# Optimization experiments

Hardware: AMD Instinct MI355X
Metric: run time of the kernel (lower is better)

## Reference

```python
import jax, jax.numpy as jnp
import numpy as np

B = 64        # number of graph segments
BASE = 384    # mean verts per segment
LMAX = 512    # pad length (counts in [256, 512])
H_DIM = 256
H_DIV = 128   # h_dim // h_dim_div
HEADS = 4
DH = H_DIV // HEADS  # 32


def _counts(seed):
    rng = np.random.default_rng(seed)
    d = rng.integers(-128, 129, B)
    d[1::2] = -d[::2]            # paired so the total is exactly B*BASE
    return (BASE + d).astype(np.int64)


def _pad_indices(counts, L):
    # Gather indices/mask mapping packed ragged tokens -> padded [B, L].
    counts = np.asarray(counts)
    off = np.concatenate([[0], np.cumsum(counts)[:-1]])
    ar = np.arange(L)[None, :]
    mask = ar < counts[:, None]
    idx = np.where(mask, off[:, None] + ar, 0)
    return idx, mask


def setup_inputs() -> dict:
    key = jax.random.key(0)
    ks = jax.random.split(key, 16)
    src_num_verts = _counts(0)
    dst_num_verts = _counts(1)
    total = B * BASE  # 24576 for both src and dst

    def w(k, shape):
        return 0.02 * jax.random.normal(k, shape, jnp.float32)

    return {
        'src_h': jax.random.normal(ks[0], (total, H_DIM), jnp.float32),
        'dst_h': jax.random.normal(ks[1], (total, H_DIM), jnp.float32),
        'src_num_verts': src_num_verts,
        'dst_num_verts': dst_num_verts,
        # 1x1 Conv1d == linear over channels
        'Wq': w(ks[2], (H_DIV, H_DIM)), 'bq': w(ks[3], (H_DIV,)),
        'Wk': w(ks[4], (H_DIV, H_DIM)), 'bk': w(ks[5], (H_DIV,)),
        'Wv': w(ks[6], (H_DIV, H_DIM)), 'bv': w(ks[7], (H_DIV,)),
        'Wm': w(ks[8], (H_DIV, H_DIV)), 'bm': w(ks[9], (H_DIV,)),
        'W1': w(ks[10], (H_DIM, H_DIM + H_DIV)), 'b1': w(ks[11], (H_DIM,)),
        'g1': 1.0 + 0.1 * jax.random.normal(ks[12], (H_DIM,), jnp.float32),
        'be1': w(ks[13], (H_DIM,)),
        'rm1': w(ks[14], (H_DIM,)),
        'rv1': jax.random.uniform(ks[15], (H_DIM,), jnp.float32, 0.5, 1.5),
        'W2': w(jax.random.fold_in(key, 100), (H_DIM, H_DIM)),
        'b2': w(jax.random.fold_in(key, 101), (H_DIM,)),
        'g2': 1.0 + 0.1 * jax.random.normal(jax.random.fold_in(key, 102), (H_DIM,), jnp.float32),
        'be2': w(jax.random.fold_in(key, 103), (H_DIM,)),
        'rm2': w(jax.random.fold_in(key, 104), (H_DIM,)),
        'rv2': jax.random.uniform(jax.random.fold_in(key, 105), (H_DIM,), jnp.float32, 0.5, 1.5),
    }


def _bn(x, g, b, rm, rv):
    # BatchNorm1d in eval mode (running stats)
    return (x - rm) / jnp.sqrt(rv + 1e-5) * g + b


def reference(src_h, dst_h, src_num_verts, dst_num_verts,
              Wq, bq, Wk, bk, Wv, bv, Wm, bm,
              W1, b1, g1, be1, rm1, rv1,
              W2, b2, g2, be2, rm2, rv2):
    didx, dmask = _pad_indices(dst_num_verts, LMAX)
    sidx, smask = _pad_indices(src_num_verts, LMAX)

    # fused projections over all packed tokens (1x1 conv == matmul)
    q = src_h_proj = dst_h @ Wq.T + bq        # [Nd, H_DIV]
    k = src_h @ Wk.T + bk                     # [Ns, H_DIV]
    v = src_h @ Wv.T + bv

    # pad to block-diagonal batched form; channel c = d*HEADS + h per torch view
    qp = q[didx].reshape(B, LMAX, DH, HEADS)
    kp = k[sidx].reshape(B, LMAX, DH, HEADS)
    vp = v[sidx].reshape(B, LMAX, DH, HEADS)

    scores = jnp.einsum('bndh,bmdh->bhnm', qp, kp) / (DH ** 0.5)
    scores = jnp.where(jnp.asarray(smask)[:, None, None, :], scores, -1e9)
    attn = jax.nn.softmax(scores, axis=-1)
    msg = jnp.einsum('bhnm,bmdh->bndh', attn, vp).reshape(B, LMAX, H_DIV)
    msg = msg @ Wm.T + bm                     # merge conv

    bb, ii = np.nonzero(dmask)                # unpad back to packed layout
    h_msg = msg[bb, ii]                       # [Nd, H_DIV]

    x = jnp.concatenate([dst_h, h_msg], axis=-1)
    x = _bn(x @ W1.T + b1, g1, be1, rm1, rv1)
    x = jax.nn.relu(x)
    x = _bn(x @ W2.T + b2, g2, be2, rm2, rv2)
    return dst_h + x
```

## Files before the change

### kernel.cpp

```cpp
#include <hip/hip_runtime.h>
#include <hip/hip_bf16.h>
#include <math.h>

#define B_SEG 64
#define HDIM 256
#define HDIV 128
#define NHEADS 4
#define DH 32
#define KSTR 40
#define VSTR 520
#define PSTR 136
#define QSC 0.17677669529663687f

typedef unsigned short u16;
typedef unsigned int u32;

typedef __attribute__((ext_vector_type(8))) short s8v;
typedef __attribute__((ext_vector_type(4))) float f4v;

__device__ __forceinline__ u16 f2bf(float f) {
    u32 v;
    __builtin_memcpy(&v, &f, 4);
    u32 r = v + 0x7fffu + ((v >> 16) & 1u);
    return (u16)(r >> 16);
}

__device__ __forceinline__ void async_cp16(const u16* g, u16* l) {
    __builtin_amdgcn_global_load_lds(
        (const __attribute__((address_space(1))) u32*)g,
        (__attribute__((address_space(3))) u32*)l, 16, 0, 0);
}

__global__ __launch_bounds__(256) void k_prep(
    const float* __restrict__ Wq, const float* __restrict__ bq,
    const float* __restrict__ Wk, const float* __restrict__ bk,
    const float* __restrict__ Wv, const float* __restrict__ bv,
    const float* __restrict__ Wm, const float* __restrict__ bm,
    const float* __restrict__ W1, const float* __restrict__ b1,
    const float* __restrict__ g1, const float* __restrict__ be1,
    const float* __restrict__ rm1, const float* __restrict__ rv1,
    const float* __restrict__ W2, const float* __restrict__ b2,
    const float* __restrict__ g2, const float* __restrict__ be2,
    const float* __restrict__ rm2, const float* __restrict__ rv2,
    const int* __restrict__ sc_raw, const int* __restrict__ dc_raw,
    const float* __restrict__ src_h, const float* __restrict__ dst_h,
    int* __restrict__ meta,
    u16* __restrict__ pWq, u16* __restrict__ pWkv,
    u16* __restrict__ pW1f, u16* __restrict__ pW2,
    float* __restrict__ bqp, float* __restrict__ bkvp,
    float* __restrict__ sc1, float* __restrict__ sh1,
    float* __restrict__ sc2, float* __restrict__ sh2,
    u16* __restrict__ srcb, u16* __restrict__ dstb, int ntot) {
    if (blockIdx.x < 1028) {
        int idx = blockIdx.x * 256 + threadIdx.x;
        if (idx < 32768) {
            int cp = idx >> 8, k = idx & 255;
            int c = ((cp & 31) << 2) | (cp >> 5);
            pWq[idx] = f2bf(Wq[c * 256 + k]);
        } else if (idx < 98304) {
            int i = idx - 32768;
            int rp = i >> 8, k = i & 255;
            int r = rp & 127;
            int c = ((r & 31) << 2) | (r >> 5);
            float v = (rp < 128) ? Wk[c * 256 + k] : Wv[c * 256 + k];
            pWkv[i] = f2bf(v);
        } else if (idx < 163840) {
            int i = idx - 98304;
            int o = i >> 8, k = i & 255;
            pW1f[o * 384 + k] = f2bf(W1[o * 384 + k]);
        } else if (idx < 196608) {
            int i = idx - 163840;
            int o = i >> 7, cp = i & 127;
            int c = ((cp & 31) << 2) | (cp >> 5);
            float acc = 0.f;
            for (int j = 0; j < 128; j++)
                acc += W1[o * 384 + 256 + j] * Wm[j * 128 + c];
            pW1f[o * 384 + 256 + cp] = f2bf(acc);
        } else if (idx < 262144) {
            int i = idx - 196608;
            pW2[i] = f2bf(W2[i]);
        } else if (idx < 263168) {
            int p = idx - 262144;
            if (p < 128) {
                int c = ((p & 31) << 2) | (p >> 5);
                bqp[p] = bq[c] * QSC;
            } else if (p < 384) {
                int r = p - 128; int rr = r & 127;
                int c = ((rr & 31) << 2) | (rr >> 5);
                bkvp[r] = (r < 128) ? bk[c] : bv[c];
            } else if (p < 640) {
                int o = p - 384;
                float bsum = 0.f;
                for (int j = 0; j < 128; j++)
                    bsum += W1[o * 384 + 256 + j] * bm[j];
                float s = g1[o] * rsqrtf(rv1[o] + 1e-5f);
                sc1[o] = s;
                sh1[o] = (b1[o] + bsum - rm1[o]) * s + be1[o];
            } else if (p < 896) {
                int o = p - 640;
                float s = g2[o] * rsqrtf(rv2[o] + 1e-5f);
                sc2[o] = s;
                sh2[o] = (b2[o] - rm2[o]) * s + be2[o];
            }
        }
    } else if (blockIdx.x == 1028) {
        if (threadIdx.x == 0) {
            bool is64 = (sc_raw[1] == 0);
            int so = 0, dofs = 0;
            for (int i = 0; i < B_SEG; i++) {
                int s = is64 ? sc_raw[2 * i] : sc_raw[i];
                int d = is64 ? dc_raw[2 * i] : dc_raw[i];
                meta[i] = s; meta[64 + i] = d;
                meta[128 + i] = so; meta[192 + i] = dofs;
                so += s; dofs += d;
            }
        }
    } else {
        int i = (blockIdx.x - 1029) * 256 + threadIdx.x;
        int half = ntot * 64;
        const float4* s;
        u16* o;
        int j = i;
        if (i < half) { s = (const float4*)src_h; o = srcb; }
        else { s = (const float4*)dst_h; o = dstb; j = i - half; }
        float4 v = s[j];
        ushort4 u = {f2bf(v.x), f2bf(v.y), f2bf(v.z), f2bf(v.w)};
        ((ushort4*)o)[j] = u;
    }
}

__device__ __forceinline__ void gemm_body(
    const u16* __restrict__ A, int lda,
    const u16* __restrict__ A2, int lda2, int K1,
    const u16* __restrict__ Bw, int K, int m0, int n0,
    const float* __restrict__ scale, const float* __restrict__ shift,
    const float* __restrict__ resid,
    void* __restrict__ Cout, int ldc, int flags,
    u16* Al, u16* Bl) {
    int tid = threadIdx.x;
    int w = tid >> 6, lane = tid & 63;
    int wm = w & 1, wn = w >> 1;
    int l15 = lane & 15, quad = lane >> 4;
    int srow = w * 32 + (lane >> 2);
    int scol = (lane & 3) << 3;
    u16* al0 = Al + w * 1024;
    u16* bl0 = Bl + w * 1024;
    f4v acc[4][4] = {};

    for (int k0 = 0; k0 < K; k0 += 32) {
        const u16* Ag; int aL, acol;
        if (k0 < K1) { Ag = A; aL = lda; acol = k0; }
        else { Ag = A2; aL = lda2; acol = k0 - K1; }
        async_cp16(&Ag[(size_t)(m0 + srow) * aL + acol + scol], al0);
        async_cp16(&Ag[(size_t)(m0 + srow + 16) * aL + acol + scol], al0 + 512);
        async_cp16(&Bw[(size_t)(n0 + srow) * K + k0 + scol], bl0);
        async_cp16(&Bw[(size_t)(n0 + srow + 16) * K + k0 + scol], bl0 + 512);
        __syncthreads();
        s8v af[4], bf[4];
#pragma unroll
        for (int i = 0; i < 4; i++)
            af[i] = *(const s8v*)(&Al[(wm * 64 + i * 16 + l15) * 32 + quad * 8]);
#pragma unroll
        for (int j = 0; j < 4; j++)
            bf[j] = *(const s8v*)(&Bl[(wn * 64 + j * 16 + l15) * 32 + quad * 8]);
#pragma unroll
        for (int i = 0; i < 4; i++)
#pragma unroll
            for (int j = 0; j < 4; j++)
                acc[i][j] = __builtin_amdgcn_mfma_f32_16x16x32_bf16(
                    af[i], bf[j], acc[i][j], 0, 0, 0);
        __syncthreads();
    }
#pragma unroll
    for (int i = 0; i < 4; i++) {
#pragma unroll
        for (int j = 0; j < 4; j++) {
            int n = n0 + wn * 64 + j * 16 + l15;
            float sc = scale ? scale[n] : 1.f;
            float sh = shift ? shift[n] : 0.f;
#pragma unroll
            for (int r = 0; r < 4; r++) {
                int m = m0 + wm * 64 + i * 16 + quad * 4 + r;
                float v = acc[i][j][r];
                if (flags & 4) v *= QSC;
                v = v * sc + sh;
                if (flags & 1) v = fmaxf(v, 0.f);
                if (resid) v += resid[(size_t)m * 256 + n];
                if (flags & 2) ((float*)Cout)[(size_t)m * ldc + n] = v;
                else ((u16*)Cout)[(size_t)m * ldc + n] = f2bf(v);
            }
        }
    }
}

__global__ __launch_bounds__(256) void k_qkv(
    const u16* __restrict__ dstb, const u16* __restrict__ srcb,
    const u16* __restrict__ pWq, const u16* __restrict__ pWkv,
    const float* __restrict__ bqp, const float* __restrict__ bkvp,
    u16* __restrict__ qb, u16* __restrict__ kvb) {
    __shared__ u16 Al[4096];
    __shared__ u16 Bl[4096];
    int m0 = blockIdx.x * 128;
    if (blockIdx.y == 0)
        gemm_body(dstb, 256, dstb, 256, 256, pWq, 256, m0, 0,
                  nullptr, bqp, nullptr, qb, 128, 4, Al, Bl);
    else
        gemm_body(srcb, 256, srcb, 256, 256, pWkv, 256, m0, (blockIdx.y - 1) * 128,
                  nullptr, bkvp, nullptr, kvb, 256, 0, Al, Bl);
}

__global__ __launch_bounds__(256) void k_mlp(
    const u16* __restrict__ dstb, const u16* __restrict__ msgb,
    const u16* __restrict__ pW1f, const u16* __restrict__ pW2,
    const float* __restrict__ sc1, const float* __restrict__ sh1,
    const float* __restrict__ sc2, const float* __restrict__ sh2,
    const float* __restrict__ dst_h, float* __restrict__ out) {
    __shared__ u16 Al[64 * 32];
    __shared__ u16 Bl[256 * 32];
    __shared__ u16 X1[64 * 256];
    int m0 = blockIdx.x * 64;
    int tid = threadIdx.x;
    int w = tid >> 6, lane = tid & 63;
    int wm = w & 1, wn = w >> 1;
    int l15 = lane & 15, quad = lane >> 4;
    int srow = w * 16 + (lane >> 2);
    int scol = (lane & 3) << 3;
    u16* al0 = Al + w * 512;
    f4v acc[2][8];

#pragma unroll
    for (int i = 0; i < 2; i++)
#pragma unroll
        for (int j = 0; j < 8; j++) acc[i][j] = (f4v){0.f, 0.f, 0.f, 0.f};

    for (int k0 = 0; k0 < 384; k0 += 32) {
        const u16* Ag; int aL, acol;
        if (k0 < 256) { Ag = dstb; aL = 256; acol = k0; }
        else { Ag = msgb; aL = 128; acol = k0 - 256; }
        async_cp16(&Ag[(size_t)(m0 + srow) * aL + acol + scol], al0);
#pragma unroll
        for (int c = 0; c < 4; c++)
            async_cp16(&pW1f[(size_t)(c * 64 + srow) * 384 + k0 + scol],
                       Bl + c * 2048 + w * 512);
        __syncthreads();
        s8v af[2], bf[8];
#pragma unroll
        for (int i = 0; i < 2; i++)
            af[i] = *(const s8v*)(&Al[(wm * 32 + i * 16 + l15) * 32 + quad * 8]);
#pragma unroll
        for (int j = 0; j < 8; j++)
            bf[j] = *(const s8v*)(&Bl[(wn * 128 + j * 16 + l15) * 32 + quad * 8]);
#pragma unroll
        for (int i = 0; i < 2; i++)
#pragma unroll
            for (int j = 0; j < 8; j++)
                acc[i][j] = __builtin_amdgcn_mfma_f32_16x16x32_bf16(
                    af[i], bf[j], acc[i][j], 0, 0, 0);
        __syncthreads();
    }
#pragma unroll
    for (int i = 0; i < 2; i++) {
#pragma unroll
        for (int j = 0; j < 8; j++) {
            int n = wn * 128 + j * 16 + l15;
            float sc = sc1[n], sh = sh1[n];
#pragma unroll
            for (int r = 0; r < 4; r++) {
                int row = wm * 32 + i * 16 + quad * 4 + r;
                float v = fmaxf(acc[i][j][r] * sc + sh, 0.f);
                int sl = (n >> 3) ^ (row & 7);
                X1[row * 256 + sl * 8 + (n & 7)] = f2bf(v);
            }
        }
    }
    __syncthreads();

#pragma unroll
    for (int i = 0; i < 2; i++)
#pragma unroll
        for (int j = 0; j < 8; j++) acc[i][j] = (f4v){0.f, 0.f, 0.f, 0.f};

    for (int k0 = 0; k0 < 256; k0 += 32) {
#pragma unroll
        for (int c = 0; c < 4; c++)
            async_cp16(&pW2[(size_t)(c * 64 + srow) * 256 + k0 + scol],
                       Bl + c * 2048 + w * 512);
        __syncthreads();
        s8v af[2], bf[8];
#pragma unroll
        for (int i = 0; i < 2; i++) {
            int row = wm * 32 + i * 16 + l15;
            int sl = ((k0 >> 3) + quad) ^ (row & 7);
            af[i] = *(const s8v*)(&X1[row * 256 + sl * 8]);
        }
#pragma unroll
        for (int j = 0; j < 8; j++)
            bf[j] = *(const s8v*)(&Bl[(wn * 128 + j * 16 + l15) * 32 + quad * 8]);
#pragma unroll
        for (int i = 0; i < 2; i++)
#pragma unroll
            for (int j = 0; j < 8; j++)
                acc[i][j] = __builtin_amdgcn_mfma_f32_16x16x32_bf16(
                    af[i], bf[j], acc[i][j], 0, 0, 0);
        __syncthreads();
    }
#pragma unroll
    for (int i = 0; i < 2; i++) {
#pragma unroll
        for (int j = 0; j < 8; j++) {
            int n = wn * 128 + j * 16 + l15;
            float sc = sc2[n], sh = sh2[n];
#pragma unroll
            for (int r = 0; r < 4; r++) {
                int m = m0 + wm * 32 + i * 16 + quad * 4 + r;
                float v = acc[i][j][r] * sc + sh + dst_h[(size_t)m * 256 + n];
                out[(size_t)m * 256 + n] = v;
            }
        }
    }
}

__global__ __launch_bounds__(512, 2) void k_attn(
    const u16* __restrict__ qb, const u16* __restrict__ kvb,
    const int* __restrict__ meta, u16* __restrict__ msgb) {
    extern __shared__ u16 sm[];
    u16* Kl = sm;
    u16* Vl = sm + 512 * KSTR;
    u16* Pl = Vl + 32 * VSTR;
    int b = blockIdx.x, h = blockIdx.y;
    int ns = meta[b], nd = meta[64 + b];
    int soff = meta[128 + b], doff = meta[192 + b];
    int tid = threadIdx.x, w = tid >> 6, lane = tid & 63;
    int l15 = lane & 15, quad = lane >> 4;

    {
        int m = tid;
        if (m < ns) {
            const uint4* ks = (const uint4*)&kvb[(size_t)(soff + m) * 256 + h * 32];
#pragma unroll
            for (int q4 = 0; q4 < 4; q4++)
                *(uint4*)&Kl[m * KSTR + q4 * 8] = ks[q4];
            uint4 vv[4];
            const uint4* vs = (const uint4*)&kvb[(size_t)(soff + m) * 256 + 128 + h * 32];
#pragma unroll
            for (int q4 = 0; q4 < 4; q4++) vv[q4] = vs[q4];
            const u16* pv = (const u16*)vv;
#pragma unroll
            for (int d = 0; d < 32; d++) Vl[d * VSTR + m] = pv[d];
        } else {
#pragma unroll
            for (int d = 0; d < 32; d++) Vl[d * VSTR + m] = 0;
        }
    }
    __syncthreads();

    int nt = (ns + 15) >> 4;
    int nc = (ns + 127) >> 7;
    u16* Pw = Pl + w * 16 * PSTR;

    for (int s0 = w * 16; s0 < nd; s0 += 128) {
        int qr = min(s0 + l15, nd - 1);
        s8v aq = *(const s8v*)&qb[(size_t)(doff + qr) * 128 + h * 32 + quad * 8];

        f4v e[32];
        float lsum[4] = {0.f, 0.f, 0.f, 0.f};
#pragma unroll
        for (int t = 0; t < 32; t++) {
            if (t < nt) {
                int kr = t * 16 + l15;
                s8v bk = *(const s8v*)&Kl[kr * KSTR + quad * 8];
                f4v s_ = __builtin_amdgcn_mfma_f32_16x16x32_bf16(
                    aq, bk, (f4v){0.f, 0.f, 0.f, 0.f}, 0, 0, 0);
                bool ok = kr < ns;
#pragma unroll
                for (int r = 0; r < 4; r++) {
                    float ev = ok ? __expf(s_[r]) : 0.f;
                    e[t][r] = ev;
                    lsum[r] += ev;
                }
            } else {
#pragma unroll
                for (int r = 0; r < 4; r++) e[t][r] = 0.f;
            }
        }
        float inv[4];
#pragma unroll
        for (int r = 0; r < 4; r++) {
            float s_ = lsum[r];
#pragma unroll
            for (int x = 1; x < 16; x <<= 1) s_ += __shfl_xor(s_, x, 16);
            inv[r] = 1.f / s_;
        }

        f4v oa0 = {0.f, 0.f, 0.f, 0.f}, oa1 = {0.f, 0.f, 0.f, 0.f};
#pragma unroll
        for (int c = 0; c < 4; c++) {
            if (c < nc) {
#pragma unroll
                for (int tt = 0; tt < 8; tt++)
#pragma unroll
                    for (int r = 0; r < 4; r++)
                        Pw[(quad * 4 + r) * PSTR + tt * 16 + l15] =
                            f2bf(e[c * 8 + tt][r]);
#pragma unroll
                for (int kc = 0; kc < 4; kc++) {
                    s8v ap = *(const s8v*)&Pw[l15 * PSTR + kc * 32 + quad * 8];
                    s8v bv0 = *(const s8v*)&Vl[l15 * VSTR + c * 128 + kc * 32 + quad * 8];
                    s8v bv1 = *(const s8v*)&Vl[(16 + l15) * VSTR + c * 128 + kc * 32 + quad * 8];
                    oa0 = __builtin_amdgcn_mfma_f32_16x16x32_bf16(ap, bv0, oa0, 0, 0, 0);
                    oa1 = __builtin_amdgcn_mfma_f32_16x16x32_bf16(ap, bv1, oa1, 0, 0, 0);
                }
            }
        }
#pragma unroll
        for (int r = 0; r < 4; r++) {
            int row = s0 + quad * 4 + r;
            if (row < nd) {
                size_t base = (size_t)(doff + row) * 128 + h * 32;
                msgb[base + l15] = f2bf(oa0[r] * inv[r]);
                msgb[base + 16 + l15] = f2bf(oa1[r] * inv[r]);
            }
        }
    }
}

extern "C" void kernel_launch(void* const* d_in, const int* in_sizes, int n_in,
                              void* d_out, int out_size, void* d_ws, size_t ws_size,
                              hipStream_t stream) {
    const float* src_h = (const float*)d_in[0];
    const float* dst_h = (const float*)d_in[1];
    const int* snv = (const int*)d_in[2];
    const int* dnv = (const int*)d_in[3];
    const float* Wq = (const float*)d_in[4];  const float* bq = (const float*)d_in[5];
    const float* Wk = (const float*)d_in[6];  const float* bk = (const float*)d_in[7];
    const float* Wv = (const float*)d_in[8];  const float* bv = (const float*)d_in[9];
    const float* Wm = (const float*)d_in[10]; const float* bm = (const float*)d_in[11];
    const float* W1 = (const float*)d_in[12]; const float* b1 = (const float*)d_in[13];
    const float* g1 = (const float*)d_in[14]; const float* be1 = (const float*)d_in[15];
    const float* rm1 = (const float*)d_in[16]; const float* rv1 = (const float*)d_in[17];
    const float* W2 = (const float*)d_in[18]; const float* b2 = (const float*)d_in[19];
    const float* g2 = (const float*)d_in[20]; const float* be2 = (const float*)d_in[21];
    const float* rm2 = (const float*)d_in[22]; const float* rv2 = (const float*)d_in[23];

    int ntot = out_size / HDIM;
    int mt = ntot / 128;

    char* ws = (char*)d_ws;
    int* meta = (int*)ws;
    float* bqp = (float*)(ws + 4096);
    float* bkvp = (float*)(ws + 4608);
    float* sc1 = (float*)(ws + 6144);
    float* sh1 = (float*)(ws + 7168);
    float* sc2 = (float*)(ws + 8192);
    float* sh2 = (float*)(ws + 9216);
    u16* pWq = (u16*)(ws + 16384);
    u16* pWkv = (u16*)(ws + 81920);
    u16* pW1f = (u16*)(ws + 212992);
    u16* pW2 = (u16*)(ws + 409600);
    u16* srcb = (u16*)(ws + 1048576);
    u16* dstb = (u16*)(ws + 13631488);
    u16* msgb = (u16*)(ws + 26214400);

    u16* qb = (u16*)d_out;
    u16* kvb = qb + (size_t)ntot * 128;

    hipFuncSetAttribute((const void*)k_attn,
                        hipFuncAttributeMaxDynamicSharedMemorySize, 131072);

    k_prep<<<dim3(1029 + ntot / 2), dim3(256), 0, stream>>>(
        Wq, bq, Wk, bk, Wv, bv, Wm, bm, W1, b1, g1, be1, rm1, rv1,
        W2, b2, g2, be2, rm2, rv2, snv, dnv, src_h, dst_h, meta,
        pWq, pWkv, pW1f, pW2, bqp, bkvp, sc1, sh1, sc2, sh2,
        srcb, dstb, ntot);
    k_qkv<<<dim3(mt, 3), dim3(256), 0, stream>>>(
        dstb, srcb, pWq, pWkv, bqp, bkvp, qb, kvb);
    k_attn<<<dim3(B_SEG, NHEADS), dim3(512), 109056, stream>>>(qb, kvb, meta, msgb);
    k_mlp<<<dim3(ntot / 64), dim3(256), 0, stream>>>(
        dstb, msgb, pW1f, pW2, sc1, sh1, sc2, sh2, dst_h, (float*)d_out);
}
```

Baseline: 220.5 us.

## Double attention block threads, swizzle LDS layouts, and halve MLP row tile

The attention kernel now runs 1024 threads per segment-head block, so each warp handles fewer query tiles. The padded K/V/P shared-memory strides are replaced with XOR-swizzled layouts, and the V transpose is split across two threads per key. The MLP kernel moves from 64-row to 32-row tiles, with each warp owning a 64-column slice, which doubles the grid. This is meant to raise parallelism and cut LDS bank conflicts, but the tighter launch bounds on a 1024-thread block could limit registers and cause spills in the large score array.

```diff
diff --git a/kernel.cpp b/kernel.cpp
--- a/kernel.cpp
+++ b/kernel.cpp
@@ -7,9 +7,6 @@
 #define HDIV 128
 #define NHEADS 4
 #define DH 32
-#define KSTR 40
-#define VSTR 520
-#define PSTR 136
 #define QSC 0.17677669529663687f
 
 typedef unsigned short u16;
@@ -209,51 +206,51 @@
                   nullptr, bkvp, nullptr, kvb, 256, 0, Al, Bl);
 }
 
-__global__ __launch_bounds__(256) void k_mlp(
+__global__ __launch_bounds__(256, 4) void k_mlp(
     const u16* __restrict__ dstb, const u16* __restrict__ msgb,
     const u16* __restrict__ pW1f, const u16* __restrict__ pW2,
     const float* __restrict__ sc1, const float* __restrict__ sh1,
     const float* __restrict__ sc2, const float* __restrict__ sh2,
     const float* __restrict__ dst_h, float* __restrict__ out) {
-    __shared__ u16 Al[64 * 32];
+    __shared__ u16 Al[32 * 32];
     __shared__ u16 Bl[256 * 32];
-    __shared__ u16 X1[64 * 256];
-    int m0 = blockIdx.x * 64;
+    __shared__ u16 X1[32 * 256];
+    int m0 = blockIdx.x * 32;
     int tid = threadIdx.x;
     int w = tid >> 6, lane = tid & 63;
-    int wm = w & 1, wn = w >> 1;
     int l15 = lane & 15, quad = lane >> 4;
-    int srow = w * 16 + (lane >> 2);
+    int srow = lane >> 2;
     int scol = (lane & 3) << 3;
-    u16* al0 = Al + w * 512;
-    f4v acc[2][8];
+    f4v acc[2][4];
 
 #pragma unroll
     for (int i = 0; i < 2; i++)
 #pragma unroll
-        for (int j = 0; j < 8; j++) acc[i][j] = (f4v){0.f, 0.f, 0.f, 0.f};
+        for (int j = 0; j < 4; j++) acc[i][j] = (f4v){0.f, 0.f, 0.f, 0.f};
 
     for (int k0 = 0; k0 < 384; k0 += 32) {
         const u16* Ag; int aL, acol;
         if (k0 < 256) { Ag = dstb; aL = 256; acol = k0; }
         else { Ag = msgb; aL = 128; acol = k0 - 256; }
-        async_cp16(&Ag[(size_t)(m0 + srow) * aL + acol + scol], al0);
-#pragma unroll
-        for (int c = 0; c < 4; c++)
-            async_cp16(&pW1f[(size_t)(c * 64 + srow) * 384 + k0 + scol],
-                       Bl + c * 2048 + w * 512);
-        __syncthreads();
-        s8v af[2], bf[8];
+#pragma unroll
+        for (int q = 0; q < 4; q++)
+            async_cp16(&pW1f[(size_t)(w * 64 + q * 16 + srow) * 384 + k0 + scol],
+                       Bl + (w * 64 + q * 16) * 32);
+        if (w < 2)
+            async_cp16(&Ag[(size_t)(m0 + w * 16 + srow) * aL + acol + scol],
+                       Al + w * 16 * 32);
+        __syncthreads();
+        s8v af[2], bf[4];
 #pragma unroll
         for (int i = 0; i < 2; i++)
-            af[i] = *(const s8v*)(&Al[(wm * 32 + i * 16 + l15) * 32 + quad * 8]);
-#pragma unroll
-        for (int j = 0; j < 8; j++)
-            bf[j] = *(const s8v*)(&Bl[(wn * 128 + j * 16 + l15) * 32 + quad * 8]);
+            af[i] = *(const s8v*)(&Al[(i * 16 + l15) * 32 + quad * 8]);
+#pragma unroll
+        for (int j = 0; j < 4; j++)
+            bf[j] = *(const s8v*)(&Bl[(w * 64 + j * 16 + l15) * 32 + quad * 8]);
 #pragma unroll
         for (int i = 0; i < 2; i++)
 #pragma unroll
-            for (int j = 0; j < 8; j++)
+            for (int j = 0; j < 4; j++)
                 acc[i][j] = __builtin_amdgcn_mfma_f32_16x16x32_bf16(
                     af[i], bf[j], acc[i][j], 0, 0, 0);
         __syncthreads();
@@ -261,15 +258,14 @@
 #pragma unroll
     for (int i = 0; i < 2; i++) {
 #pragma unroll
-        for (int j = 0; j < 8; j++) {
-            int n = wn * 128 + j * 16 + l15;
+        for (int j = 0; j < 4; j++) {
+            int n = w * 64 + j * 16 + l15;
             float sc = sc1[n], sh = sh1[n];
 #pragma unroll
             for (int r = 0; r < 4; r++) {
-                int row = wm * 32 + i * 16 + quad * 4 + r;
+                int row = i * 16 + quad * 4 + r;
                 float v = fmaxf(acc[i][j][r] * sc + sh, 0.f);
-                int sl = (n >> 3) ^ (row & 7);
-                X1[row * 256 + sl * 8 + (n & 7)] = f2bf(v);
+                X1[row * 256 + ((n >> 3) ^ (row & 7)) * 8 + (n & 7)] = f2bf(v);
             }
         }
     }
@@ -278,28 +274,28 @@
 #pragma unroll
     for (int i = 0; i < 2; i++)
 #pragma unroll
-        for (int j = 0; j < 8; j++) acc[i][j] = (f4v){0.f, 0.f, 0.f, 0.f};
+        for (int j = 0; j < 4; j++) acc[i][j] = (f4v){0.f, 0.f, 0.f, 0.f};
 
     for (int k0 = 0; k0 < 256; k0 += 32) {
 #pragma unroll
-        for (int c = 0; c < 4; c++)
-            async_cp16(&pW2[(size_t)(c * 64 + srow) * 256 + k0 + scol],
-                       Bl + c * 2048 + w * 512);
-        __syncthreads();
-        s8v af[2], bf[8];
+        for (int q = 0; q < 4; q++)
+            async_cp16(&pW2[(size_t)(w * 64 + q * 16 + srow) * 256 + k0 + scol],
+                       Bl + (w * 64 + q * 16) * 32);
+        __syncthreads();
+        s8v af[2], bf[4];
 #pragma unroll
         for (int i = 0; i < 2; i++) {
-            int row = wm * 32 + i * 16 + l15;
-            int sl = ((k0 >> 3) + quad) ^ (row & 7);
-            af[i] = *(const s8v*)(&X1[row * 256 + sl * 8]);
-        }
-#pragma unroll
-        for (int j = 0; j < 8; j++)
-            bf[j] = *(const s8v*)(&Bl[(wn * 128 + j * 16 + l15) * 32 + quad * 8]);
+            int row = i * 16 + l15;
+            af[i] = *(const s8v*)(
+                &X1[row * 256 + (((k0 >> 3) + quad) ^ (row & 7)) * 8]);
+        }
+#pragma unroll
+        for (int j = 0; j < 4; j++)
+            bf[j] = *(const s8v*)(&Bl[(w * 64 + j * 16 + l15) * 32 + quad * 8]);
 #pragma unroll
         for (int i = 0; i < 2; i++)
 #pragma unroll
-            for (int j = 0; j < 8; j++)
+            for (int j = 0; j < 4; j++)
                 acc[i][j] = __builtin_amdgcn_mfma_f32_16x16x32_bf16(
                     af[i], bf[j], acc[i][j], 0, 0, 0);
         __syncthreads();
@@ -307,12 +303,12 @@
 #pragma unroll
     for (int i = 0; i < 2; i++) {
 #pragma unroll
-        for (int j = 0; j < 8; j++) {
-            int n = wn * 128 + j * 16 + l15;
+        for (int j = 0; j < 4; j++) {
+            int n = w * 64 + j * 16 + l15;
             float sc = sc2[n], sh = sh2[n];
 #pragma unroll
             for (int r = 0; r < 4; r++) {
-                int m = m0 + wm * 32 + i * 16 + quad * 4 + r;
+                int m = m0 + i * 16 + quad * 4 + r;
                 float v = acc[i][j][r] * sc + sh + dst_h[(size_t)m * 256 + n];
                 out[(size_t)m * 256 + n] = v;
             }
@@ -320,13 +316,13 @@
     }
 }
 
-__global__ __launch_bounds__(512, 2) void k_attn(
+__global__ __launch_bounds__(1024, 4) void k_attn(
     const u16* __restrict__ qb, const u16* __restrict__ kvb,
     const int* __restrict__ meta, u16* __restrict__ msgb) {
     extern __shared__ u16 sm[];
     u16* Kl = sm;
-    u16* Vl = sm + 512 * KSTR;
-    u16* Pl = Vl + 32 * VSTR;
+    u16* Vl = sm + 16384;
+    u16* Pl = sm + 32768;
     int b = blockIdx.x, h = blockIdx.y;
     int ns = meta[b], nd = meta[64 + b];
     int soff = meta[128 + b], doff = meta[192 + b];
@@ -338,27 +334,36 @@
         if (m < ns) {
             const uint4* ks = (const uint4*)&kvb[(size_t)(soff + m) * 256 + h * 32];
 #pragma unroll
-            for (int q4 = 0; q4 < 4; q4++)
-                *(uint4*)&Kl[m * KSTR + q4 * 8] = ks[q4];
-            uint4 vv[4];
-            const uint4* vs = (const uint4*)&kvb[(size_t)(soff + m) * 256 + 128 + h * 32];
-#pragma unroll
-            for (int q4 = 0; q4 < 4; q4++) vv[q4] = vs[q4];
+            for (int s = 0; s < 4; s++)
+                *(uint4*)&Kl[m * 32 + (s ^ ((m >> 1) & 3)) * 8] = ks[s];
+        }
+        int vm = tid >> 1, d0 = (tid & 1) * 16;
+        if (vm < ns) {
+            uint4 vv[2];
+            const uint4* vs =
+                (const uint4*)&kvb[(size_t)(soff + vm) * 256 + 128 + h * 32 + d0];
+            vv[0] = vs[0]; vv[1] = vs[1];
             const u16* pv = (const u16*)vv;
 #pragma unroll
-            for (int d = 0; d < 32; d++) Vl[d * VSTR + m] = pv[d];
+            for (int dd = 0; dd < 16; dd++) {
+                int d = d0 + dd;
+                Vl[d * 512 + ((vm >> 3) ^ (d & 7)) * 8 + (vm & 7)] = pv[dd];
+            }
         } else {
 #pragma unroll
-            for (int d = 0; d < 32; d++) Vl[d * VSTR + m] = 0;
+            for (int dd = 0; dd < 16; dd++) {
+                int d = d0 + dd;
+                Vl[d * 512 + ((vm >> 3) ^ (d & 7)) * 8 + (vm & 7)] = 0;
+            }
         }
     }
     __syncthreads();
 
     int nt = (ns + 15) >> 4;
     int nc = (ns + 127) >> 7;
-    u16* Pw = Pl + w * 16 * PSTR;
-
-    for (int s0 = w * 16; s0 < nd; s0 += 128) {
+    u16* Pw = Pl + w * 2048;
+
+    for (int s0 = w * 16; s0 < nd; s0 += 256) {
         int qr = min(s0 + l15, nd - 1);
         s8v aq = *(const s8v*)&qb[(size_t)(doff + qr) * 128 + h * 32 + quad * 8];
 
@@ -368,7 +373,7 @@
         for (int t = 0; t < 32; t++) {
             if (t < nt) {
                 int kr = t * 16 + l15;
-                s8v bk = *(const s8v*)&Kl[kr * KSTR + quad * 8];
+                s8v bk = *(const s8v*)&Kl[kr * 32 + (quad ^ ((l15 >> 1) & 3)) * 8];
                 f4v s_ = __builtin_amdgcn_mfma_f32_16x16x32_bf16(
                     aq, bk, (f4v){0.f, 0.f, 0.f, 0.f}, 0, 0, 0);
                 bool ok = kr < ns;
@@ -399,14 +404,18 @@
 #pragma unroll
                 for (int tt = 0; tt < 8; tt++)
 #pragma unroll
-                    for (int r = 0; r < 4; r++)
-                        Pw[(quad * 4 + r) * PSTR + tt * 16 + l15] =
+                    for (int r = 0; r < 4; r++) {
+                        int row = quad * 4 + r;
+                        int slot = tt * 2 + (l15 >> 3);
+                        Pw[row * 128 + (slot ^ row) * 8 + (l15 & 7)] =
                             f2bf(e[c * 8 + tt][r]);
+                    }
 #pragma unroll
                 for (int kc = 0; kc < 4; kc++) {
-                    s8v ap = *(const s8v*)&Pw[l15 * PSTR + kc * 32 + quad * 8];
-                    s8v bv0 = *(const s8v*)&Vl[l15 * VSTR + c * 128 + kc * 32 + quad * 8];
-                    s8v bv1 = *(const s8v*)&Vl[(16 + l15) * VSTR + c * 128 + kc * 32 + quad * 8];
+                    s8v ap = *(const s8v*)&Pw[l15 * 128 + ((kc * 4 + quad) ^ l15) * 8];
+                    int vslot = c * 16 + kc * 4 + quad;
+                    s8v bv0 = *(const s8v*)&Vl[l15 * 512 + (vslot ^ (l15 & 7)) * 8];
+                    s8v bv1 = *(const s8v*)&Vl[(16 + l15) * 512 + (vslot ^ (l15 & 7)) * 8];
                     oa0 = __builtin_amdgcn_mfma_f32_16x16x32_bf16(ap, bv0, oa0, 0, 0, 0);
                     oa1 = __builtin_amdgcn_mfma_f32_16x16x32_bf16(ap, bv1, oa1, 0, 0, 0);
                 }
@@ -474,7 +483,7 @@
         srcb, dstb, ntot);
     k_qkv<<<dim3(mt, 3), dim3(256), 0, stream>>>(
         dstb, srcb, pWq, pWkv, bqp, bkvp, qb, kvb);
-    k_attn<<<dim3(B_SEG, NHEADS), dim3(512), 109056, stream>>>(qb, kvb, meta, msgb);
-    k_mlp<<<dim3(ntot / 64), dim3(256), 0, stream>>>(
+    k_attn<<<dim3(B_SEG, NHEADS), dim3(1024), 131072, stream>>>(qb, kvb, meta, msgb);
+    k_mlp<<<dim3(ntot / 32), dim3(256), 0, stream>>>(
         dstb, msgb, pW1f, pW2, sc1, sh1, sc2, sh2, dst_h, (float*)d_out);
 }
```

Measured after the change: 306.6 us. 39.0% more time.
